# Optimization experiments

Hardware: AMD Instinct MI355X
Metric: run time of the kernel (lower is better)

Reference implementation:

```python
import jax, jax.numpy as jnp
import numpy as np

EPS = 1e-5
COMMITMENT_WEIGHT = 1.0


def setup_inputs() -> dict:
    key = jax.random.key(0)
    k1, k2 = jax.random.split(key)
    x = jax.random.normal(k1, (4, 4096, 128), dtype=jnp.float32)
    codebook = jax.random.normal(k2, (8192, 128), dtype=jnp.float32)
    return {"x": x, "codebook": codebook}


def _layernorm(x):
    # LayerNorm over last dim, elementwise_affine=False, eps=1e-5
    mu = jnp.mean(x, axis=-1, keepdims=True)
    var = jnp.mean(jnp.square(x - mu), axis=-1, keepdims=True)
    return (x - mu) * jax.lax.rsqrt(var + EPS)


def reference(x, codebook):
    b, n, d = x.shape
    xn = _layernorm(x)                      # [b, n, d]
    flat = xn.reshape(b * n, d)             # [bn, d]
    x2 = jnp.sum(flat * flat, axis=-1, keepdims=True)          # [bn, 1]
    e2 = jnp.sum(codebook * codebook, axis=-1)                  # [K]
    dots = jnp.einsum('nd,kd->nk', flat, codebook)              # [bn, K]
    distances = x2 - 2.0 * dots + e2[None, :]                   # [bn, K]
    embed_ind = jnp.argmin(distances, axis=-1)                  # [bn]
    quantize = codebook[embed_ind].reshape(b, n, d)             # gather
    embed_ind = embed_ind.reshape(b, n)
    loss = jnp.mean(jnp.square(quantize - xn)) * COMMITMENT_WEIGHT
    # straight-through
    quantize_st = xn + jax.lax.stop_gradient(quantize - xn)
    return (quantize_st, embed_ind, loss)
```

## Files before the change

### kernel.cpp

```cpp
#include <hip/hip_runtime.h>
#include <hip/hip_fp16.h>
#include <math.h>

typedef _Float16 half8  __attribute__((ext_vector_type(8)));
typedef _Float16 half2v __attribute__((ext_vector_type(2)));
typedef float   floatx4 __attribute__((ext_vector_type(4)));

#define ROWS   16384
#define DIM    128
#define KCODES 8192
#define NSPLIT 8
#define MTILE  512
#define NT     64
#define NCHUNK ((KCODES / NSPLIT) / NT)
#define NCAND  (2 * NSPLIT)

__device__ __forceinline__ void async_copy16(const _Float16* src, _Float16* dst_lds) {
  __builtin_amdgcn_global_load_lds((const __attribute__((address_space(1))) void*)src,
                                   (__attribute__((address_space(3))) void*)dst_lds,
                                   16, 0, 0);
}

__global__ __launch_bounds__(256) void prep_codebook(
    const float* __restrict__ cb, _Float16* __restrict__ ehg,
    _Float16* __restrict__ elg, float* __restrict__ e2g)
{
  int tid = threadIdx.x;
  int L = tid & 63;
  int row = blockIdx.x * 4 + (tid >> 6);
  const float2* cr = (const float2*)(cb + (size_t)row * DIM);
  float2 v = cr[L];
  float s2 = v.x * v.x + v.y * v.y;
  #pragma unroll
  for (int m = 1; m < 64; m <<= 1) s2 += __shfl_xor(s2, m);
  if (L == 0) e2g[row] = -0.5f * s2;
  _Float16 h0 = (_Float16)v.x, h1 = (_Float16)v.y;
  half2v hi = {h0, h1};
  half2v lo = {(_Float16)(v.x - (float)h0), (_Float16)(v.y - (float)h1)};
  ((half2v*)(ehg + (size_t)row * DIM))[L] = hi;
  ((half2v*)(elg + (size_t)row * DIM))[L] = lo;
}

__global__ __launch_bounds__(512, 1) void argmin_kernel(
    const float* __restrict__ x, const _Float16* __restrict__ ehg,
    const _Float16* __restrict__ elg, const float* __restrict__ e2g,
    float* __restrict__ b1p, int* __restrict__ i1p,
    float* __restrict__ b2p, int* __restrict__ i2p)
{
  __shared__ _Float16 ebuf[2][2][64][128];

  int tid = threadIdx.x;
  int w   = tid >> 6;
  int L   = tid & 63;
  int c   = L & 15;
  int q   = L >> 4;

  int bx = blockIdx.x;
  int mt = bx & (ROWS / MTILE - 1);
  int ns = bx >> 5;

  int rowbase = mt * MTILE + w * 64;

  half8 ah[4][4];

  #pragma unroll
  for (int g = 0; g < 4; ++g) {
    const float* xr = x + (size_t)(rowbase + g * 16 + c) * DIM;
    float v[32];
    #pragma unroll
    for (int ks = 0; ks < 4; ++ks) {
      float4 p0 = *(const float4*)(xr + ks * 32 + q * 8);
      float4 p1 = *(const float4*)(xr + ks * 32 + q * 8 + 4);
      v[ks*8+0] = p0.x; v[ks*8+1] = p0.y; v[ks*8+2] = p0.z; v[ks*8+3] = p0.w;
      v[ks*8+4] = p1.x; v[ks*8+5] = p1.y; v[ks*8+6] = p1.z; v[ks*8+7] = p1.w;
    }
    float s = 0.f;
    #pragma unroll
    for (int i = 0; i < 32; ++i) s += v[i];
    s += __shfl_xor(s, 16); s += __shfl_xor(s, 32);
    float mu = s * (1.0f / 128.0f);
    float s2 = 0.f;
    #pragma unroll
    for (int i = 0; i < 32; ++i) { float d = v[i] - mu; s2 += d * d; }
    s2 += __shfl_xor(s2, 16); s2 += __shfl_xor(s2, 32);
    float rstd = 1.0f / sqrtf(s2 * (1.0f / 128.0f) + 1e-5f);
    #pragma unroll
    for (int ks = 0; ks < 4; ++ks)
      #pragma unroll
      for (int j = 0; j < 8; ++j)
        ah[g][ks][j] = (_Float16)((v[ks*8+j] - mu) * rstd);
  }

  float b1[4][4], b2[4][4]; int i1[4][4], i2[4][4];
  #pragma unroll
  for (int g = 0; g < 4; ++g)
    #pragma unroll
    for (int r = 0; r < 4; ++r) {
      b1[g][r] = -3.4e38f; b2[g][r] = -3.4e38f;
      i1[g][r] = 0; i2[g][r] = 0;
    }

  int code0 = ns * (KCODES / NSPLIT);
  _Float16* lbase = &ebuf[0][0][0][0];

  auto stage = [&](int ch, int p) {
    int cbase = code0 + ch * NT;
    _Float16* lb = lbase + (size_t)p * 2 * 64 * 128;
    #pragma unroll
    for (int it = 0; it < 4; ++it) {
      int cid = it * 512 + tid;
      int arr = cid >> 10;
      int lc  = cid & 1023;
      int n   = lc >> 4;
      int kcs = lc & 15;
      int kc  = kcs ^ (n & 7);
      const _Float16* g = (arr ? elg : ehg) + (size_t)(cbase + n) * DIM + kc * 8;
      async_copy16(g, lb + (size_t)cid * 8);
    }
  };

  stage(0, 0);
  __syncthreads();

  for (int ch = 0; ch < NCHUNK; ++ch) {
    int p = ch & 1;
    int cbase = code0 + ch * NT;
    if (ch + 1 < NCHUNK) stage(ch + 1, p ^ 1);

    float e2h[4];
    #pragma unroll
    for (int s = 0; s < 4; ++s) e2h[s] = e2g[cbase + s * 16 + c];

    #pragma unroll
    for (int s = 0; s < 4; ++s) {
      int n = s * 16 + c;
      half8 bh[4], bl[4];
      #pragma unroll
      for (int ks = 0; ks < 4; ++ks) {
        int slot = ((ks * 4 + q) ^ (c & 7)) * 8;
        bh[ks] = *(const half8*)&ebuf[p][0][n][slot];
        bl[ks] = *(const half8*)&ebuf[p][1][n][slot];
      }
      int nn = cbase + n;
      #pragma unroll
      for (int g = 0; g < 4; ++g) {
        floatx4 acc = {e2h[s], e2h[s], e2h[s], e2h[s]};
        #pragma unroll
        for (int ks = 0; ks < 4; ++ks) {
          acc = __builtin_amdgcn_mfma_f32_16x16x32_f16(ah[g][ks], bh[ks], acc, 0, 0, 0);
          acc = __builtin_amdgcn_mfma_f32_16x16x32_f16(ah[g][ks], bl[ks], acc, 0, 0, 0);
        }
        #pragma unroll
        for (int r = 0; r < 4; ++r) {
          float t = acc[r];
          bool gt1 = t > b1[g][r];
          bool gt2 = t > b2[g][r];
          b2[g][r] = gt1 ? b1[g][r] : (gt2 ? t  : b2[g][r]);
          i2[g][r] = gt1 ? i1[g][r] : (gt2 ? nn : i2[g][r]);
          b1[g][r] = gt1 ? t  : b1[g][r];
          i1[g][r] = gt1 ? nn : i1[g][r];
        }
      }
    }
    __syncthreads();
  }

  #pragma unroll
  for (int m = 1; m < 16; m <<= 1)
    #pragma unroll
    for (int g = 0; g < 4; ++g)
      #pragma unroll
      for (int r = 0; r < 4; ++r) {
        float ob1 = __shfl_xor(b1[g][r], m); int oi1 = __shfl_xor(i1[g][r], m);
        float ob2 = __shfl_xor(b2[g][r], m); int oi2 = __shfl_xor(i2[g][r], m);
        if (ob1 > b1[g][r]) {
          float nb2 = (b1[g][r] >= ob2) ? b1[g][r] : ob2;
          int   ni2 = (b1[g][r] >= ob2) ? i1[g][r] : oi2;
          b1[g][r] = ob1; i1[g][r] = oi1;
          b2[g][r] = nb2; i2[g][r] = ni2;
        } else {
          float nb2 = (ob1 >= b2[g][r]) ? ob1 : b2[g][r];
          int   ni2 = (ob1 >= b2[g][r]) ? oi1 : i2[g][r];
          b2[g][r] = nb2; i2[g][r] = ni2;
        }
      }
  if (c == 0) {
    #pragma unroll
    for (int g = 0; g < 4; ++g)
      #pragma unroll
      for (int r = 0; r < 4; ++r) {
        int row = rowbase + g * 16 + q * 4 + r;
        b1p[(size_t)row * NSPLIT + ns] = b1[g][r];
        i1p[(size_t)row * NSPLIT + ns] = i1[g][r];
        b2p[(size_t)row * NSPLIT + ns] = b2[g][r];
        i2p[(size_t)row * NSPLIT + ns] = i2[g][r];
      }
  }
}

__global__ __launch_bounds__(256) void gather_loss_kernel(
    const float* __restrict__ x, const float* __restrict__ cb,
    const float* __restrict__ e2g,
    const int* __restrict__ i1p, const int* __restrict__ i2p,
    float* __restrict__ out_q, float* __restrict__ out_ind,
    float* __restrict__ row_loss)
{
  int tid = threadIdx.x;
  int L = tid & 63;
  int row = blockIdx.x * 4 + (tid >> 6);

  int ci = 0;
  if (L < 8)       ci = i1p[(size_t)row * NSPLIT + L];
  else if (L < 16) ci = i2p[(size_t)row * NSPLIT + (L - 8)];

  float2 xv = ((const float2*)(x + (size_t)row * DIM))[L];
  float s = xv.x + xv.y;
  #pragma unroll
  for (int m = 1; m < 64; m <<= 1) s += __shfl_xor(s, m);
  float mu = s * (1.0f / 128.0f);
  float dx = xv.x - mu, dy = xv.y - mu;
  float s2 = dx * dx + dy * dy;
  #pragma unroll
  for (int m = 1; m < 64; m <<= 1) s2 += __shfl_xor(s2, m);
  float rstd = 1.0f / sqrtf(s2 * (1.0f / 128.0f) + 1e-5f);
  float xn0 = dx * rstd, xn1 = dy * rstd;

  int idxs[NCAND];
  #pragma unroll
  for (int k = 0; k < NCAND; ++k) idxs[k] = __shfl(ci, k);
  float2 evs[NCAND];
  float  e2s[NCAND];
  #pragma unroll
  for (int k = 0; k < NCAND; ++k) {
    evs[k] = ((const float2*)(cb + (size_t)idxs[k] * DIM))[L];
    e2s[k] = e2g[idxs[k]];
  }

  float bestT = -3.4e38f; int bestI = 0x7fffffff;
  #pragma unroll
  for (int k = 0; k < NCAND; ++k) {
    float pp = xn0 * evs[k].x + xn1 * evs[k].y;
    #pragma unroll
    for (int m = 1; m < 64; m <<= 1) pp += __shfl_xor(pp, m);
    float t = pp + e2s[k];
    int idx = idxs[k];
    if (t > bestT || (t == bestT && idx < bestI)) { bestT = t; bestI = idx; }
  }

  float2 qv = ((const float2*)(cb + (size_t)bestI * DIM))[L];
  ((float2*)out_q)[(size_t)row * 64 + L] = qv;
  float e0 = qv.x - xn0, e1 = qv.y - xn1;
  float le = e0 * e0 + e1 * e1;
  #pragma unroll
  for (int m = 1; m < 64; m <<= 1) le += __shfl_xor(le, m);
  if (L == 0) {
    row_loss[row] = le;
    out_ind[row] = (float)bestI;
  }
}

__global__ __launch_bounds__(1024) void loss_reduce_kernel(
    const float* __restrict__ row_loss, float* __restrict__ out_loss)
{
  __shared__ float sm[1024];
  int tid = threadIdx.x;
  float s = 0.f;
  for (int i = tid; i < ROWS; i += 1024) s += row_loss[i];
  sm[tid] = s; __syncthreads();
  for (int st = 512; st > 0; st >>= 1) {
    if (tid < st) sm[tid] += sm[tid + st];
    __syncthreads();
  }
  if (tid == 0) *out_loss = sm[0] * (1.0f / (float)(ROWS * DIM));
}

extern "C" void kernel_launch(void* const* d_in, const int* in_sizes, int n_in,
                              void* d_out, int out_size, void* d_ws, size_t ws_size,
                              hipStream_t stream)
{
  const float* x  = (const float*)d_in[0];
  const float* cb = (const float*)d_in[1];

  char* ws = (char*)d_ws;
  _Float16* ehg      = (_Float16*)(ws + 0);
  _Float16* elg      = (_Float16*)(ws + 2097152);
  float*    e2g      = (float*)   (ws + 4194304);
  float*    b1p      = (float*)   (ws + 4227072);
  int*      i1p      = (int*)     (ws + 4751360);
  float*    b2p      = (float*)   (ws + 5275648);
  int*      i2p      = (int*)     (ws + 5799936);
  float*    row_loss = (float*)   (ws + 6324224);

  float* out_q    = (float*)d_out;
  float* out_ind  = out_q + (size_t)ROWS * DIM;
  float* out_loss = out_ind + ROWS;

  prep_codebook<<<KCODES / 4, 256, 0, stream>>>(cb, ehg, elg, e2g);
  argmin_kernel<<<(ROWS / MTILE) * NSPLIT, 512, 0, stream>>>(x, ehg, elg, e2g, b1p, i1p, b2p, i2p);
  gather_loss_kernel<<<ROWS / 4, 256, 0, stream>>>(x, cb, e2g, i1p, i2p, out_q, out_ind, row_loss);
  loss_reduce_kernel<<<1, 1024, 0, stream>>>(row_loss, out_loss);
}
```

Before: 177.1 us.

## Precompute fp16 normalized rows, shrink argmin tiles for occupancy, parallelize candidate rescoring

After: 373.8 us. +111.1%, slower.

```diff
diff --git a/kernel.cpp b/kernel.cpp
--- a/kernel.cpp
+++ b/kernel.cpp
@@ -9,9 +9,9 @@
 #define ROWS   16384
 #define DIM    128
 #define KCODES 8192
-#define NSPLIT 8
-#define MTILE  512
-#define NT     64
+#define NSPLIT 16
+#define MTILE  256
+#define NT     32
 #define NCHUNK ((KCODES / NSPLIT) / NT)
 #define NCAND  (2 * NSPLIT)
 
@@ -21,33 +21,49 @@
                                    16, 0, 0);
 }
 
-__global__ __launch_bounds__(256) void prep_codebook(
-    const float* __restrict__ cb, _Float16* __restrict__ ehg,
-    _Float16* __restrict__ elg, float* __restrict__ e2g)
+__global__ __launch_bounds__(256) void prep_kernel(
+    const float* __restrict__ cb, const float* __restrict__ x,
+    _Float16* __restrict__ ehg, _Float16* __restrict__ elg,
+    float* __restrict__ e2g, _Float16* __restrict__ xnh)
 {
   int tid = threadIdx.x;
   int L = tid & 63;
-  int row = blockIdx.x * 4 + (tid >> 6);
-  const float2* cr = (const float2*)(cb + (size_t)row * DIM);
-  float2 v = cr[L];
-  float s2 = v.x * v.x + v.y * v.y;
-  #pragma unroll
-  for (int m = 1; m < 64; m <<= 1) s2 += __shfl_xor(s2, m);
-  if (L == 0) e2g[row] = -0.5f * s2;
-  _Float16 h0 = (_Float16)v.x, h1 = (_Float16)v.y;
-  half2v hi = {h0, h1};
-  half2v lo = {(_Float16)(v.x - (float)h0), (_Float16)(v.y - (float)h1)};
-  ((half2v*)(ehg + (size_t)row * DIM))[L] = hi;
-  ((half2v*)(elg + (size_t)row * DIM))[L] = lo;
-}
-
-__global__ __launch_bounds__(512, 1) void argmin_kernel(
-    const float* __restrict__ x, const _Float16* __restrict__ ehg,
+  int bx = blockIdx.x;
+  if (bx < KCODES / 4) {
+    int row = bx * 4 + (tid >> 6);
+    float2 v = ((const float2*)(cb + (size_t)row * DIM))[L];
+    float s2 = v.x * v.x + v.y * v.y;
+    #pragma unroll
+    for (int m = 1; m < 64; m <<= 1) s2 += __shfl_xor(s2, m);
+    if (L == 0) e2g[row] = -0.5f * s2;
+    _Float16 h0 = (_Float16)v.x, h1 = (_Float16)v.y;
+    half2v hi = {h0, h1};
+    half2v lo = {(_Float16)(v.x - (float)h0), (_Float16)(v.y - (float)h1)};
+    ((half2v*)(ehg + (size_t)row * DIM))[L] = hi;
+    ((half2v*)(elg + (size_t)row * DIM))[L] = lo;
+  } else {
+    int row = (bx - KCODES / 4) * 4 + (tid >> 6);
+    float2 xv = ((const float2*)(x + (size_t)row * DIM))[L];
+    float s = xv.x + xv.y;
+    #pragma unroll
+    for (int m = 1; m < 64; m <<= 1) s += __shfl_xor(s, m);
+    float mu = s * (1.0f / 128.0f);
+    float dx = xv.x - mu, dy = xv.y - mu;
+    float s2 = dx * dx + dy * dy;
+    #pragma unroll
+    for (int m = 1; m < 64; m <<= 1) s2 += __shfl_xor(s2, m);
+    float rstd = 1.0f / sqrtf(s2 * (1.0f / 128.0f) + 1e-5f);
+    half2v hv = {(_Float16)(dx * rstd), (_Float16)(dy * rstd)};
+    ((half2v*)(xnh + (size_t)row * DIM))[L] = hv;
+  }
+}
+
+__global__ __launch_bounds__(256, 4) void argmin_kernel(
+    const _Float16* __restrict__ xnh, const _Float16* __restrict__ ehg,
     const _Float16* __restrict__ elg, const float* __restrict__ e2g,
-    float* __restrict__ b1p, int* __restrict__ i1p,
-    float* __restrict__ b2p, int* __restrict__ i2p)
-{
-  __shared__ _Float16 ebuf[2][2][64][128];
+    int* __restrict__ i1p, int* __restrict__ i2p)
+{
+  __shared__ _Float16 ebuf[2][2][NT][128];
 
   int tid = threadIdx.x;
   int w   = tid >> 6;
@@ -57,38 +73,17 @@
 
   int bx = blockIdx.x;
   int mt = bx & (ROWS / MTILE - 1);
-  int ns = bx >> 5;
+  int ns = bx >> 6;
 
   int rowbase = mt * MTILE + w * 64;
 
   half8 ah[4][4];
-
   #pragma unroll
   for (int g = 0; g < 4; ++g) {
-    const float* xr = x + (size_t)(rowbase + g * 16 + c) * DIM;
-    float v[32];
-    #pragma unroll
-    for (int ks = 0; ks < 4; ++ks) {
-      float4 p0 = *(const float4*)(xr + ks * 32 + q * 8);
-      float4 p1 = *(const float4*)(xr + ks * 32 + q * 8 + 4);
-      v[ks*8+0] = p0.x; v[ks*8+1] = p0.y; v[ks*8+2] = p0.z; v[ks*8+3] = p0.w;
-      v[ks*8+4] = p1.x; v[ks*8+5] = p1.y; v[ks*8+6] = p1.z; v[ks*8+7] = p1.w;
-    }
-    float s = 0.f;
-    #pragma unroll
-    for (int i = 0; i < 32; ++i) s += v[i];
-    s += __shfl_xor(s, 16); s += __shfl_xor(s, 32);
-    float mu = s * (1.0f / 128.0f);
-    float s2 = 0.f;
-    #pragma unroll
-    for (int i = 0; i < 32; ++i) { float d = v[i] - mu; s2 += d * d; }
-    s2 += __shfl_xor(s2, 16); s2 += __shfl_xor(s2, 32);
-    float rstd = 1.0f / sqrtf(s2 * (1.0f / 128.0f) + 1e-5f);
+    const _Float16* xr = xnh + (size_t)(rowbase + g * 16 + c) * DIM;
     #pragma unroll
     for (int ks = 0; ks < 4; ++ks)
-      #pragma unroll
-      for (int j = 0; j < 8; ++j)
-        ah[g][ks][j] = (_Float16)((v[ks*8+j] - mu) * rstd);
+      ah[g][ks] = *(const half8*)(xr + ks * 32 + q * 8);
   }
 
   float b1[4][4], b2[4][4]; int i1[4][4], i2[4][4];
@@ -105,12 +100,12 @@
 
   auto stage = [&](int ch, int p) {
     int cbase = code0 + ch * NT;
-    _Float16* lb = lbase + (size_t)p * 2 * 64 * 128;
+    _Float16* lb = lbase + (size_t)p * 2 * NT * 128;
     #pragma unroll
     for (int it = 0; it < 4; ++it) {
-      int cid = it * 512 + tid;
-      int arr = cid >> 10;
-      int lc  = cid & 1023;
+      int cid = it * 256 + tid;
+      int arr = cid >> 9;
+      int lc  = cid & 511;
       int n   = lc >> 4;
       int kcs = lc & 15;
       int kc  = kcs ^ (n & 7);
@@ -120,19 +115,22 @@
   };
 
   stage(0, 0);
+  float e2c[2], e2n[2];
+  e2c[0] = e2g[code0 + c];
+  e2c[1] = e2g[code0 + 16 + c];
   __syncthreads();
 
   for (int ch = 0; ch < NCHUNK; ++ch) {
     int p = ch & 1;
     int cbase = code0 + ch * NT;
-    if (ch + 1 < NCHUNK) stage(ch + 1, p ^ 1);
-
-    float e2h[4];
-    #pragma unroll
-    for (int s = 0; s < 4; ++s) e2h[s] = e2g[cbase + s * 16 + c];
-
-    #pragma unroll
-    for (int s = 0; s < 4; ++s) {
+    if (ch + 1 < NCHUNK) {
+      stage(ch + 1, p ^ 1);
+      e2n[0] = e2g[cbase + NT + c];
+      e2n[1] = e2g[cbase + NT + 16 + c];
+    }
+
+    #pragma unroll
+    for (int s = 0; s < 2; ++s) {
       int n = s * 16 + c;
       half8 bh[4], bl[4];
       #pragma unroll
@@ -144,7 +142,7 @@
       int nn = cbase + n;
       #pragma unroll
       for (int g = 0; g < 4; ++g) {
-        floatx4 acc = {e2h[s], e2h[s], e2h[s], e2h[s]};
+        floatx4 acc = {e2c[s], e2c[s], e2c[s], e2c[s]};
         #pragma unroll
         for (int ks = 0; ks < 4; ++ks) {
           acc = __builtin_amdgcn_mfma_f32_16x16x32_f16(ah[g][ks], bh[ks], acc, 0, 0, 0);
@@ -163,6 +161,7 @@
       }
     }
     __syncthreads();
+    e2c[0] = e2n[0]; e2c[1] = e2n[1];
   }
 
   #pragma unroll
@@ -190,9 +189,7 @@
       #pragma unroll
       for (int r = 0; r < 4; ++r) {
         int row = rowbase + g * 16 + q * 4 + r;
-        b1p[(size_t)row * NSPLIT + ns] = b1[g][r];
         i1p[(size_t)row * NSPLIT + ns] = i1[g][r];
-        b2p[(size_t)row * NSPLIT + ns] = b2[g][r];
         i2p[(size_t)row * NSPLIT + ns] = i2[g][r];
       }
   }
@@ -209,9 +206,13 @@
   int L = tid & 63;
   int row = blockIdx.x * 4 + (tid >> 6);
 
+  int k  = L & 31;
+  int qd = L >> 5;
+
   int ci = 0;
-  if (L < 8)       ci = i1p[(size_t)row * NSPLIT + L];
-  else if (L < 16) ci = i2p[(size_t)row * NSPLIT + (L - 8)];
+  if (L < 16)      ci = i1p[(size_t)row * NSPLIT + L];
+  else if (L < 32) ci = i2p[(size_t)row * NSPLIT + (L - 16)];
+  int idxk = __shfl(ci, k);
 
   float2 xv = ((const float2*)(x + (size_t)row * DIM))[L];
   float s = xv.x + xv.y;
@@ -223,39 +224,38 @@
   #pragma unroll
   for (int m = 1; m < 64; m <<= 1) s2 += __shfl_xor(s2, m);
   float rstd = 1.0f / sqrtf(s2 * (1.0f / 128.0f) + 1e-5f);
+
+  const float4* xr4 = (const float4*)(x  + (size_t)row  * DIM);
+  const float4* er4 = (const float4*)(cb + (size_t)idxk * DIM);
+  float p = 0.f;
+  #pragma unroll
+  for (int j = 0; j < 16; ++j) {
+    float4 a = xr4[qd * 16 + j];
+    float4 e = er4[qd * 16 + j];
+    p += (a.x - mu) * e.x + (a.y - mu) * e.y + (a.z - mu) * e.z + (a.w - mu) * e.w;
+  }
+  p *= rstd;
+  p += __shfl_xor(p, 32);
+  float t = p + e2g[idxk];
+
+  int bi = idxk;
+  #pragma unroll
+  for (int m = 1; m < 32; m <<= 1) {
+    float ot = __shfl_xor(t, m);
+    int   oi = __shfl_xor(bi, m);
+    if (ot > t || (ot == t && oi < bi)) { t = ot; bi = oi; }
+  }
+
+  float2 qv = ((const float2*)(cb + (size_t)bi * DIM))[L];
+  ((float2*)out_q)[(size_t)row * 64 + L] = qv;
   float xn0 = dx * rstd, xn1 = dy * rstd;
-
-  int idxs[NCAND];
-  #pragma unroll
-  for (int k = 0; k < NCAND; ++k) idxs[k] = __shfl(ci, k);
-  float2 evs[NCAND];
-  float  e2s[NCAND];
-  #pragma unroll
-  for (int k = 0; k < NCAND; ++k) {
-    evs[k] = ((const float2*)(cb + (size_t)idxs[k] * DIM))[L];
-    e2s[k] = e2g[idxs[k]];
-  }
-
-  float bestT = -3.4e38f; int bestI = 0x7fffffff;
-  #pragma unroll
-  for (int k = 0; k < NCAND; ++k) {
-    float pp = xn0 * evs[k].x + xn1 * evs[k].y;
-    #pragma unroll
-    for (int m = 1; m < 64; m <<= 1) pp += __shfl_xor(pp, m);
-    float t = pp + e2s[k];
-    int idx = idxs[k];
-    if (t > bestT || (t == bestT && idx < bestI)) { bestT = t; bestI = idx; }
-  }
-
-  float2 qv = ((const float2*)(cb + (size_t)bestI * DIM))[L];
-  ((float2*)out_q)[(size_t)row * 64 + L] = qv;
   float e0 = qv.x - xn0, e1 = qv.y - xn1;
   float le = e0 * e0 + e1 * e1;
   #pragma unroll
   for (int m = 1; m < 64; m <<= 1) le += __shfl_xor(le, m);
   if (L == 0) {
     row_loss[row] = le;
-    out_ind[row] = (float)bestI;
+    out_ind[row] = (float)bi;
   }
 }
 
@@ -285,18 +285,18 @@
   _Float16* ehg      = (_Float16*)(ws + 0);
   _Float16* elg      = (_Float16*)(ws + 2097152);
   float*    e2g      = (float*)   (ws + 4194304);
-  float*    b1p      = (float*)   (ws + 4227072);
-  int*      i1p      = (int*)     (ws + 4751360);
-  float*    b2p      = (float*)   (ws + 5275648);
-  int*      i2p      = (int*)     (ws + 5799936);
+  int*      i1p      = (int*)     (ws + 4227072);
+  int*      i2p      = (int*)     (ws + 5275648);
   float*    row_loss = (float*)   (ws + 6324224);
 
   float* out_q    = (float*)d_out;
   float* out_ind  = out_q + (size_t)ROWS * DIM;
   float* out_loss = out_ind + ROWS;
 
-  prep_codebook<<<KCODES / 4, 256, 0, stream>>>(cb, ehg, elg, e2g);
-  argmin_kernel<<<(ROWS / MTILE) * NSPLIT, 512, 0, stream>>>(x, ehg, elg, e2g, b1p, i1p, b2p, i2p);
+  _Float16* xnh = (_Float16*)out_q;
+
+  prep_kernel<<<KCODES / 4 + ROWS / 4, 256, 0, stream>>>(cb, x, ehg, elg, e2g, xnh);
+  argmin_kernel<<<(ROWS / MTILE) * NSPLIT, 256, 0, stream>>>(xnh, ehg, elg, e2g, i1p, i2p);
   gather_loss_kernel<<<ROWS / 4, 256, 0, stream>>>(x, cb, e2g, i1p, i2p, out_q, out_ind, row_loss);
   loss_reduce_kernel<<<1, 1024, 0, stream>>>(row_loss, out_loss);
 }
```
